# Optimization experiments

Measured on AMD Instinct MI355X. Metric: run time of the kernel, lower is better.

Reference implementation:

```python
import jax, jax.numpy as jnp
import numpy as np

W_CHAMFER = (1.0, 1.0, 1.0)
W_LAPLACE = 0.5
W_MOVE = 0.1
W_EDGE = 0.1
W_NORMAL = 1.6e-4
W_CONST = 1.0
LAP_CONST = (0.2, 1.0, 1.0)
EPS = 1e-12


def _normalize(x):
    # F.normalize(x, dim=-1): x / max(||x||, eps)
    n = jnp.sqrt(jnp.sum(x * x, axis=-1, keepdims=True))
    return x / jnp.maximum(n, EPS)


def _pairwise_sq(x, y):
    # x: (B,N,3), y: (B,M,3) -> (B,N,M) squared distances, GEMM form
    x2 = jnp.sum(x * x, -1)
    y2 = jnp.sum(y * y, -1)
    xy = jnp.einsum('bnd,bmd->bnm', x, y)
    return x2[:, :, None] + y2[:, None, :] - 2.0 * xy


def _laplace_coord(pts, lap_idx):
    # pts: (B,V,3); lap_idx: (V,10) = [8 neighbor idx (-1 invalid), self, count]
    idx = lap_idx[:, :8]
    mask = idx < 0
    safe = jnp.where(mask, 0, idx)
    nbrs = pts[:, safe]                                  # (B,V,8,3)
    nbrs = jnp.where(mask[None, :, :, None], 0.0, nbrs)
    count = lap_idx[:, -1].astype(pts.dtype)
    return pts - nbrs.sum(2) / count[None, :, None]


def setup_inputs():
    key = jax.random.key(0)
    B, M = 2, 8192
    Vs = (642, 2562, 10242)
    Es = (1920, 7680, 30720)
    ks = jax.random.split(key, 3 + 4 * 3)
    inp = {}
    inp['gt_coord'] = jax.random.normal(ks[0], (B, M, 3), jnp.float32)
    inp['gt_normal'] = _normalize(jax.random.normal(ks[1], (B, M, 3), jnp.float32))
    for i, (V, E) in enumerate(zip(Vs, Es)):
        k0, k1, k2, k3 = ks[3 + 4 * i], ks[4 + 4 * i], ks[5 + 4 * i], ks[6 + 4 * i]
        inp[f'pred_coord_{i}'] = jax.random.normal(k0, (B, V, 3), jnp.float32)
        inp[f'pred_before_{i}'] = inp[f'pred_coord_{i}'] + 0.05 * jax.random.normal(k1, (B, V, 3), jnp.float32)
        inp[f'edges_{i}'] = jax.random.randint(k2, (E, 2), 0, V)
        nbr = jax.random.randint(k3, (V, 8), 0, V)
        nbr = nbr.at[:, 6:].set(-1)                      # 6 valid neighbors, 2 invalid slots
        self_idx = jnp.arange(V)[:, None]
        count = jnp.full((V, 1), 6)
        inp[f'laplace_idx_{i}'] = jnp.concatenate([nbr, self_idx, count], axis=1)
    return inp


def reference(pred_coord_0, pred_coord_1, pred_coord_2, pred_before_0, pred_before_1, pred_before_2, gt_coord, gt_normal, laplace_idx_0, laplace_idx_1, laplace_idx_2, edges_0, edges_1, edges_2):
    preds = (pred_coord_0, pred_coord_1, pred_coord_2)
    befores = (pred_before_0, pred_before_1, pred_before_2)
    laps = (laplace_idx_0, laplace_idx_1, laplace_idx_2)
    edges_all = (edges_0, edges_1, edges_2)
    chamfer_loss = 0.0
    edge_loss = 0.0
    normal_loss = 0.0
    lap_loss = 0.0
    move_loss = 0.0
    for i in range(3):
        pred, before, lap_idx, edges = preds[i], befores[i], laps[i], edges_all[i]
        # shared pairwise distance matrix for chamfer + knn (original recomputes)
        d = _pairwise_sq(pred, gt_coord)                 # (B,V,M)
        chamfer_loss = chamfer_loss + W_CHAMFER[i] * (jnp.mean(jnp.min(d, axis=1)) + jnp.mean(jnp.min(d, axis=2)))
        knn_idx = jnp.argmin(d, axis=2)                  # (B,V): nearest gt per pred pt
        e0, e1 = edges[:, 0], edges[:, 1]
        evec = _normalize(pred[:, e0] - pred[:, e1])     # (B,E,3)
        # faithful to torch: knn.idx.flatten() then index_select -> only batch-0
        # indices ever selected since edge ids < V
        sel = knn_idx.reshape(-1)[e0]
        nrm = _normalize(gt_normal[:, sel])              # (B,E,3)
        normal_loss = normal_loss + jnp.mean(jnp.abs(jnp.sum(evec * nrm, axis=2)))
        edge_loss = edge_loss + 3.0 * jnp.mean((pred[:, e0] - pred[:, e1]) ** 2)
        l1 = _laplace_coord(before, lap_idx)
        l2 = _laplace_coord(pred, lap_idx)
        lap_loss = lap_loss + LAP_CONST[i] * 3.0 * jnp.mean((l1 - l2) ** 2)
        if i > 0:
            move_loss = move_loss + LAP_CONST[i] * 3.0 * jnp.mean((before - pred) ** 2)
    loss = chamfer_loss + W_LAPLACE * lap_loss + W_MOVE * move_loss + W_EDGE * edge_loss + W_NORMAL * normal_loss
    return W_CONST * loss
```

## Files before the change

kernel.cpp:

```cpp
#include <hip/hip_runtime.h>


#define DEV __device__ __forceinline__

DEV unsigned int ford(float f) {
    unsigned int u = __float_as_uint(f);
    return (u & 0x80000000u) ? ~u : (u | 0x80000000u);
}
DEV float funord(unsigned int o) {
    unsigned int u = (o & 0x80000000u) ? (o ^ 0x80000000u) : ~o;
    return __uint_as_float(u);
}
DEV unsigned long long umin64(unsigned long long a, unsigned long long b) { return a < b ? a : b; }

DEV float blockReduceSum256(float v) {
    #pragma unroll
    for (int o = 32; o > 0; o >>= 1) v += __shfl_down(v, o, 64);
    __shared__ float red4[4];
    int wid = threadIdx.x >> 6;
    if ((threadIdx.x & 63) == 0) red4[wid] = v;
    __syncthreads();
    return (threadIdx.x == 0) ? (red4[0] + red4[1] + red4[2] + red4[3]) : 0.0f;
}

template<bool STORE, bool ARGMIN>
DEV void roleA(int a, const float* p0, const float* p1, const float* p2,
               const float* gt, char* ws, char* smem)
{
    const int b = ARGMIN ? 0 : 1;
    int vtG = a >> 5, mc = a & 31;
    int lvl, vtL, V; const float* predL;
    if (vtG == 0)      { lvl = 0; vtL = 0;       V = 642;   predL = p0; }
    else if (vtG < 4)  { lvl = 1; vtL = vtG - 1; V = 2562;  predL = p1; }
    else               { lvl = 2; vtL = vtG - 4; V = 10242; predL = p2; }
    int tid = threadIdx.x, lane = tid & 63, w = tid >> 6;
    float4* SG = (float4*)smem;
    int mbase = mc << 8;
    {
        int m = mbase + tid;
        const float* gp = gt + ((size_t)b * 8192 + m) * 3;
        float gx = gp[0], gy = gp[1], gz = gp[2];
        SG[tid] = make_float4(-2.f * gx, -2.f * gy, -2.f * gz, fmaf(gx, gx, fmaf(gy, gy, gz * gz)));
    }
    float px[14], py[14], pz[14];
    #pragma unroll
    for (int r = 0; r < 14; r++) {
        int vr = vtL * 896 + r * 64 + lane;
        int v = vr - (vr >= V ? V : 0);
        const float* pp = predL + ((size_t)b * V + v) * 3;
        px[r] = pp[0]; py[r] = pp[1]; pz[r] = pp[2];
    }
    __syncthreads();
    if (ARGMIN) {
        float best[14]; int bi[14];
        #pragma unroll
        for (int r = 0; r < 14; r++) { best[r] = 3.0e38f; bi[r] = 0; }
        #pragma unroll 4
        for (int i = 0; i < 64; i++) {
            int j = (w << 6) + i;
            float4 q = SG[j];
            int cand = mbase + j;
            #pragma unroll
            for (int r = 0; r < 14; r++) {
                float d = fmaf(q.x, px[r], fmaf(q.y, py[r], fmaf(q.z, pz[r], q.w)));
                if (d < best[r]) { best[r] = d; bi[r] = cand; }
            }
        }
        unsigned long long* RED = (unsigned long long*)(smem + 4096);
        #pragma unroll
        for (int r = 0; r < 14; r++)
            RED[w * 896 + r * 64 + lane] = ((unsigned long long)ford(best[r]) << 32) | (unsigned)bi[r];
        __syncthreads();
        for (int s = tid; s < 896; s += 256) {
            unsigned long long mm = umin64(umin64(RED[s], RED[s + 896]),
                                           umin64(RED[s + 1792], RED[s + 2688]));
            if (STORE) {
                ((unsigned long long*)(ws + 54808))[((size_t)(vtG * 896 + s)) * 32 + mc] = mm;
            } else {
                int vr = vtL * 896 + s; int v = vr - (vr >= V ? V : 0);
                int lvlOff = (lvl == 0) ? 0 : (lvl == 1 ? 642 : 3204);
                atomicMin((unsigned long long*)(ws + 54808) + (lvlOff + v), mm);
            }
        }
    } else {
        float best[14];
        #pragma unroll
        for (int r = 0; r < 14; r++) best[r] = 3.0e38f;
        #pragma unroll 2
        for (int i = 0; i < 64; i += 2) {
            int j = (w << 6) + i;
            float4 q0 = SG[j], q1 = SG[j + 1];
            #pragma unroll
            for (int r = 0; r < 14; r++) {
                float d0 = fmaf(q0.x, px[r], fmaf(q0.y, py[r], fmaf(q0.z, pz[r], q0.w)));
                float d1 = fmaf(q1.x, px[r], fmaf(q1.y, py[r], fmaf(q1.z, pz[r], q1.w)));
                best[r] = fminf(fminf(best[r], d0), d1);
            }
        }
        unsigned* RED = (unsigned*)(smem + 4096);
        #pragma unroll
        for (int r = 0; r < 14; r++)
            RED[w * 896 + r * 64 + lane] = ford(best[r]);
        __syncthreads();
        for (int s = tid; s < 896; s += 256) {
            unsigned mm = min(min(RED[s], RED[s + 896]), min(RED[s + 1792], RED[s + 2688]));
            if (STORE) {
                ((unsigned*)(ws + 3724824))[((size_t)(vtG * 896 + s)) * 32 + mc] = mm;
            } else {
                int vr = vtL * 896 + s; int v = vr - (vr >= V ? V : 0);
                int lvlOff = (lvl == 0) ? 0 : (lvl == 1 ? 642 : 3204);
                atomicMin((unsigned*)(ws + 162376) + (lvlOff + v), mm);
            }
        }
    }
}

template<bool STORE>
DEV void roleB(int i, const float* p0, const float* p1, const float* p2,
               const float* gt, char* ws, char* smem)
{
    int lvl, V, cc, t, lvlB, baseB;
    if (i < 32)       { lvl = 0; V = 642;   cc = 2;  t = i;       lvlB = 0;     baseB = 0; }
    else if (i < 128) { lvl = 1; V = 2562;  cc = 6;  t = i - 32;  lvlB = 16384; baseB = 32768; }
    else              { lvl = 2; V = 10242; cc = 21; t = i - 128; lvlB = 32768; baseB = 131072; }
    const float* predL = lvl == 0 ? p0 : (lvl == 1 ? p1 : p2);
    int c = t % cc; int rest = t / cc; int mt = rest & 7; int b = rest >> 3;
    int tid = threadIdx.x, lane = tid & 63, w = tid >> 6;
    float4* SP = (float4*)smem;
    int vbase = c * 512;
    #pragma unroll
    for (int k = 0; k < 2; k++) {
        int j = tid + k * 256, v = vbase + j;
        if (v < V) {
            const float* pp = predL + ((size_t)b * V + v) * 3;
            float x = pp[0], y = pp[1], z = pp[2];
            SP[j] = make_float4(-2.f * x, -2.f * y, -2.f * z, fmaf(x, x, fmaf(y, y, z * z)));
        } else SP[j] = make_float4(0.f, 0.f, 0.f, 3.0e38f);
    }
    float gx[16], gy[16], gz[16];
    #pragma unroll
    for (int r = 0; r < 16; r++) {
        int m = mt * 1024 + r * 64 + lane;
        const float* gp = gt + ((size_t)b * 8192 + m) * 3;
        gx[r] = gp[0]; gy[r] = gp[1]; gz[r] = gp[2];
    }
    __syncthreads();
    float best[16];
    #pragma unroll
    for (int r = 0; r < 16; r++) best[r] = 3.0e38f;
    #pragma unroll 2
    for (int i2 = 0; i2 < 128; i2 += 2) {
        int j = (w << 7) + i2;
        float4 q0 = SP[j], q1 = SP[j + 1];
        #pragma unroll
        for (int r = 0; r < 16; r++) {
            float d0 = fmaf(q0.x, gx[r], fmaf(q0.y, gy[r], fmaf(q0.z, gz[r], q0.w)));
            float d1 = fmaf(q1.x, gx[r], fmaf(q1.y, gy[r], fmaf(q1.z, gz[r], q1.w)));
            best[r] = fminf(fminf(best[r], d0), d1);
        }
    }
    unsigned* RED = (unsigned*)(smem + 8192);
    #pragma unroll
    for (int r = 0; r < 16; r++)
        RED[w * 1024 + r * 64 + lane] = ford(best[r]);
    __syncthreads();
    for (int s = tid; s < 1024; s += 256) {
        unsigned mm = min(min(RED[s], RED[s + 1024]), min(RED[s + 2048], RED[s + 3072]));
        int m = mt * 1024 + s;
        if (STORE) ((unsigned*)(ws + 5559832))[baseB + (size_t)((b << 13) + m) * cc + c] = mm;
        else       atomicMin((unsigned*)(ws + 216160) + (lvlB + (b << 13) + m), mm);
    }
}

template<bool STORE>
__global__ __launch_bounds__(256, 3) void kMega(
    const float* __restrict__ p0, const float* __restrict__ p1, const float* __restrict__ p2,
    const float* __restrict__ b0p, const float* __restrict__ b1p, const float* __restrict__ b2p,
    const int* __restrict__ l0, const int* __restrict__ l1, const int* __restrict__ l2,
    const float* __restrict__ gt, char* ws)
{
    extern __shared__ char smem[];
    int bid = blockIdx.x;
    if (bid == 0 && threadIdx.x == 0) { *(float*)ws = 0.f; *(unsigned*)(ws + 4) = 0u; }
    if (bid < 128) {
        float c = 0.0f;
        int idx = bid * 256 + threadIdx.x;
        if (idx < 26892) {
            int level, V, t;
            const float *pred, *bef; const int* lap;
            if (idx < 1284)      { level = 0; V = 642;   pred = p0; bef = b0p; lap = l0; t = idx; }
            else if (idx < 6408) { level = 1; V = 2562;  pred = p1; bef = b1p; lap = l1; t = idx - 1284; }
            else                 { level = 2; V = 10242; pred = p2; bef = b2p; lap = l2; t = idx - 6408; }
            int b = t / V;
            int v = t - b * V;
            const float* P  = pred + ((size_t)b * V + v) * 3;
            const float* Bf = bef  + ((size_t)b * V + v) * 3;
            float dx = Bf[0] - P[0], dy = Bf[1] - P[1], dz = Bf[2] - P[2];
            float sx = 0.f, sy = 0.f, sz = 0.f;
            const int* L = lap + v * 10;
            #pragma unroll
            for (int j = 0; j < 8; j++) {
                int n = L[j];
                if (n >= 0) {
                    const float* Pn = pred + ((size_t)b * V + n) * 3;
                    const float* Bn = bef  + ((size_t)b * V + n) * 3;
                    sx += Bn[0] - Pn[0]; sy += Bn[1] - Pn[1]; sz += Bn[2] - Pn[2];
                }
            }
            float invc = 1.0f / (float)L[9];
            float lx = dx - sx * invc, ly = dy - sy * invc, lz = dz - sz * invc;
            float sl = fmaf(lx, lx, fmaf(ly, ly, lz * lz));
            float sm = fmaf(dx, dx, fmaf(dy, dy, dz * dz));
            float lapc = (level == 0) ? 0.2f : 1.0f;
            float iBV = 1.0f / (2.0f * (float)V);
            c = sl * (0.5f * lapc * iBV) + ((level > 0) ? sm * (0.1f * lapc * iBV) : 0.0f);
        }
        c = blockReduceSum256(c);
        if (threadIdx.x == 0) ((float*)(ws + 8))[bid] = c;
    }
    else if (bid < 592)  roleB<STORE>(bid - 128, p0, p1, p2, gt, ws, smem);
    else if (bid < 1104) roleA<STORE, true >(bid - 592,  p0, p1, p2, gt, ws, smem);
    else                 roleA<STORE, false>(bid - 1104, p0, p1, p2, gt, ws, smem);
}

template<bool STORE>
__global__ __launch_bounds__(256) void kCombine(
    const float* __restrict__ p0, const float* __restrict__ p1, const float* __restrict__ p2,
    const float* __restrict__ gt, char* ws)
{
    int bid = blockIdx.x, tid = threadIdx.x;
    float c = 0.0f;
    if (bid == 304) {
        if (tid < 128) c = ((float*)(ws + 8))[tid];
    } else {
        int idx = bid * 256 + tid;
        if (idx < 28672) {
            int b = idx / 14336;
            int q = idx % 14336;
            int vtG = q / 896, s = q % 896;
            int lvl, vtL, V; const float* predL; int lvlOff; float inv;
            if (vtG == 0)     { lvl = 0; vtL = 0;       V = 642;   predL = p0; lvlOff = 0;    inv = 1.f / 1284.f; }
            else if (vtG < 4) { lvl = 1; vtL = vtG - 1; V = 2562;  predL = p1; lvlOff = 642;  inv = 1.f / 5124.f; }
            else              { lvl = 2; vtL = vtG - 4; V = 10242; predL = p2; lvlOff = 3204; inv = 1.f / 20484.f; }
            int vr = vtL * 896 + s;
            if (vr < V) {
                float d; unsigned idxm = 0;
                if (STORE) {
                    if (b == 0) {
                        const unsigned long long* P = (const unsigned long long*)(ws + 54808)
                                                      + ((size_t)(vtG * 896 + s)) * 32;
                        unsigned long long mm = ~0ull;
                        #pragma unroll 8
                        for (int k = 0; k < 32; k++) mm = umin64(mm, P[k]);
                        d = funord((unsigned)(mm >> 32)); idxm = (unsigned)mm;
                    } else {
                        const unsigned* P = (const unsigned*)(ws + 3724824)
                                            + ((size_t)(vtG * 896 + s)) * 32;
                        unsigned mm = 0xFFFFFFFFu;
                        #pragma unroll 8
                        for (int k = 0; k < 32; k++) mm = min(mm, P[k]);
                        d = funord(mm);
                    }
                } else {
                    if (b == 0) {
                        unsigned long long mm = ((unsigned long long*)(ws + 54808))[lvlOff + vr];
                        d = funord((unsigned)(mm >> 32)); idxm = (unsigned)mm;
                    } else {
                        d = funord(((unsigned*)(ws + 162376))[lvlOff + vr]);
                    }
                }
                const float* pp = predL + ((size_t)b * V + vr) * 3;
                c = (d + fmaf(pp[0], pp[0], fmaf(pp[1], pp[1], pp[2] * pp[2]))) * inv;
                if (b == 0) ((int*)(ws + 1024))[lvlOff + vr] = (int)idxm;
            }
        } else if (idx < 77824) {
            int jj = idx - 28672;
            int lvl = jj >> 14, r = jj & 16383;
            int cc = lvl == 0 ? 2 : (lvl == 1 ? 6 : 21);
            int baseB = lvl == 0 ? 0 : (lvl == 1 ? 32768 : 131072);
            float d;
            if (STORE) {
                const unsigned* P = (const unsigned*)(ws + 5559832) + baseB + (size_t)r * cc;
                unsigned mm = 0xFFFFFFFFu;
                for (int k = 0; k < cc; k++) mm = min(mm, P[k]);
                d = funord(mm);
            } else {
                d = funord(((const unsigned*)(ws + 216160))[(lvl << 14) + r]);
            }
            const float* gp = gt + (size_t)r * 3;
            c = (d + fmaf(gp[0], gp[0], fmaf(gp[1], gp[1], gp[2] * gp[2]))) * (1.f / 16384.f);
        }
    }
    c = blockReduceSum256(c);
    if (tid == 0) atomicAdd((float*)ws, c);
}

__global__ __launch_bounds__(256) void kEdgeOut(
    const float* __restrict__ p0, const float* __restrict__ p1, const float* __restrict__ p2,
    const int* __restrict__ e0p, const int* __restrict__ e1p, const int* __restrict__ e2p,
    const float* __restrict__ gtn, char* ws, float* __restrict__ out)
{
    const int* knn = (const int*)(ws + 1024);
    int idx = blockIdx.x * 256 + threadIdx.x;
    float c = 0.0f;
    {
        int E, V, lvlOff, t;
        const float* pred; const int* edges;
        if (idx < 3840)       { E = 1920;  V = 642;   lvlOff = 0;    pred = p0; edges = e0p; t = idx; }
        else if (idx < 19200) { E = 7680;  V = 2562;  lvlOff = 642;  pred = p1; edges = e1p; t = idx - 3840; }
        else                  { E = 30720; V = 10242; lvlOff = 3204; pred = p2; edges = e2p; t = idx - 19200; }
        int b = t / E;
        int e = t % E;
        int a0 = edges[e * 2 + 0];
        int a1 = edges[e * 2 + 1];
        const float* P = pred + (size_t)b * V * 3;
        float dx = P[a0 * 3 + 0] - P[a1 * 3 + 0];
        float dy = P[a0 * 3 + 1] - P[a1 * 3 + 1];
        float dz = P[a0 * 3 + 2] - P[a1 * 3 + 2];
        float sq = fmaf(dx, dx, fmaf(dy, dy, dz * dz));
        float inv = 1.0f / fmaxf(sqrtf(sq), 1e-12f);
        int sel = knn[lvlOff + a0];
        const float* nr = gtn + ((size_t)b * 8192 + sel) * 3;
        float nx = nr[0], ny = nr[1], nz = nr[2];
        float invn = 1.0f / fmaxf(sqrtf(fmaf(nx, nx, fmaf(ny, ny, nz * nz))), 1e-12f);
        float dotv = fmaf(dx, nx, fmaf(dy, ny, dz * nz)) * inv * invn;
        float iBE = 1.0f / (2.0f * (float)E);
        c = sq * (0.1f * iBE) + fabsf(dotv) * (0.00016f * iBE);
    }
    c = blockReduceSum256(c);
    if (threadIdx.x == 0) {
        atomicAdd((float*)ws, c);
        __threadfence();
        unsigned t = atomicAdd((unsigned*)(ws + 4), 1u);
        if (t == 314u) out[0] = atomicAdd((float*)ws, 0.0f);
    }
}

extern "C" void kernel_launch(void* const* d_in, const int* in_sizes, int n_in,
                              void* d_out, int out_size, void* d_ws, size_t ws_size,
                              hipStream_t stream) {
    const float *gt, *gtn, *pred[3], *bef[3];
    const int *edg[3], *lapx[3];
    if (in_sizes[0] == 49152) {
        gt  = (const float*)d_in[0];
        gtn = (const float*)d_in[1];
        for (int i = 0; i < 3; i++) {
            pred[i] = (const float*)d_in[2 + 4 * i];
            bef[i]  = (const float*)d_in[3 + 4 * i];
            edg[i]  = (const int*)  d_in[4 + 4 * i];
            lapx[i] = (const int*)  d_in[5 + 4 * i];
        }
    } else {
        for (int i = 0; i < 3; i++) pred[i] = (const float*)d_in[i];
        for (int i = 0; i < 3; i++) bef[i]  = (const float*)d_in[3 + i];
        gt  = (const float*)d_in[6];
        gtn = (const float*)d_in[7];
        for (int i = 0; i < 3; i++) lapx[i] = (const int*)d_in[8 + i];
        for (int i = 0; i < 3; i++) edg[i]  = (const int*)d_in[11 + i];
    }

    char* ws = (char*)d_ws;
    bool store = ws_size >= (size_t)7460376;

    if (store) {
        kMega<true><<<1616, 256, 32768, stream>>>(pred[0], pred[1], pred[2],
                                                  bef[0], bef[1], bef[2],
                                                  lapx[0], lapx[1], lapx[2], gt, ws);
        kCombine<true><<<305, 256, 0, stream>>>(pred[0], pred[1], pred[2], gt, ws);
    } else {
        hipMemsetAsync(ws + 54808, 0xFF, 412768 - 54808, stream);
        kMega<false><<<1616, 256, 32768, stream>>>(pred[0], pred[1], pred[2],
                                                   bef[0], bef[1], bef[2],
                                                   lapx[0], lapx[1], lapx[2], gt, ws);
        kCombine<false><<<305, 256, 0, stream>>>(pred[0], pred[1], pred[2], gt, ws);
    }
    kEdgeOut<<<315, 256, 0, stream>>>(pred[0], pred[1], pred[2],
                                      edg[0], edg[1], edg[2], gtn, ws, (float*)d_out);
}
```

Before: 140.0 us.

## Use atomicMin reductions, merge combine and edge kernels, shrink roleB tiles

Drops the per-chunk partial-min store path and always reduces nearest distances with global atomicMin into a compact buffer. Folds the chamfer combine and edge/normal loss into one final kernel that reads the argmin index straight from the packed 64-bit min. roleB tiles get smaller (256 pred points), which yields more blocks, and the reduction scratch reuses the shared tile, lowering LDS so four blocks fit per CU. The cost is more atomic traffic and two memsets, in exchange for one fewer launch and less workspace traffic.

```diff
diff --git a/kernel.cpp b/kernel.cpp
--- a/kernel.cpp
+++ b/kernel.cpp
@@ -3,12 +3,18 @@
 
 #define DEV __device__ __forceinline__
 
-DEV unsigned int ford(float f) {
-    unsigned int u = __float_as_uint(f);
+#define OFF_LAP  8
+#define OFF_MA0  1024
+#define OFF_MA1  108592
+#define OFF_MB   162376
+#define MINS_END 358984
+
+DEV unsigned ford(float f) {
+    unsigned u = __float_as_uint(f);
     return (u & 0x80000000u) ? ~u : (u | 0x80000000u);
 }
-DEV float funord(unsigned int o) {
-    unsigned int u = (o & 0x80000000u) ? (o ^ 0x80000000u) : ~o;
+DEV float funord(unsigned o) {
+    unsigned u = (o & 0x80000000u) ? (o ^ 0x80000000u) : ~o;
     return __uint_as_float(u);
 }
 DEV unsigned long long umin64(unsigned long long a, unsigned long long b) { return a < b ? a : b; }
@@ -23,31 +29,31 @@
     return (threadIdx.x == 0) ? (red4[0] + red4[1] + red4[2] + red4[3]) : 0.0f;
 }
 
-template<bool STORE, bool ARGMIN>
+template<bool ARGMIN>
 DEV void roleA(int a, const float* p0, const float* p1, const float* p2,
                const float* gt, char* ws, char* smem)
 {
     const int b = ARGMIN ? 0 : 1;
     int vtG = a >> 5, mc = a & 31;
-    int lvl, vtL, V; const float* predL;
-    if (vtG == 0)      { lvl = 0; vtL = 0;       V = 642;   predL = p0; }
-    else if (vtG < 4)  { lvl = 1; vtL = vtG - 1; V = 2562;  predL = p1; }
-    else               { lvl = 2; vtL = vtG - 4; V = 10242; predL = p2; }
+    int vtL, V, lvlOff; const float* predL;
+    if (vtG == 0)     { vtL = 0;       V = 642;   predL = p0; lvlOff = 0; }
+    else if (vtG < 4) { vtL = vtG - 1; V = 2562;  predL = p1; lvlOff = 642; }
+    else              { vtL = vtG - 4; V = 10242; predL = p2; lvlOff = 3204; }
     int tid = threadIdx.x, lane = tid & 63, w = tid >> 6;
     float4* SG = (float4*)smem;
     int mbase = mc << 8;
     {
-        int m = mbase + tid;
-        const float* gp = gt + ((size_t)b * 8192 + m) * 3;
+        const float* gp = gt + ((size_t)(b * 8192 + mbase + tid)) * 3;
         float gx = gp[0], gy = gp[1], gz = gp[2];
-        SG[tid] = make_float4(-2.f * gx, -2.f * gy, -2.f * gz, fmaf(gx, gx, fmaf(gy, gy, gz * gz)));
+        SG[tid] = make_float4(-2.f * gx, -2.f * gy, -2.f * gz,
+                              fmaf(gx, gx, fmaf(gy, gy, gz * gz)));
     }
     float px[14], py[14], pz[14];
     #pragma unroll
     for (int r = 0; r < 14; r++) {
         int vr = vtL * 896 + r * 64 + lane;
         int v = vr - (vr >= V ? V : 0);
-        const float* pp = predL + ((size_t)b * V + v) * 3;
+        const float* pp = predL + ((size_t)(b * V + v)) * 3;
         px[r] = pp[0]; py[r] = pp[1]; pz[r] = pp[2];
     }
     __syncthreads();
@@ -66,21 +72,18 @@
                 if (d < best[r]) { best[r] = d; bi[r] = cand; }
             }
         }
-        unsigned long long* RED = (unsigned long long*)(smem + 4096);
+        __syncthreads();
+        unsigned long long* RED = (unsigned long long*)smem;
         #pragma unroll
         for (int r = 0; r < 14; r++)
             RED[w * 896 + r * 64 + lane] = ((unsigned long long)ford(best[r]) << 32) | (unsigned)bi[r];
         __syncthreads();
+        unsigned long long* MA0 = (unsigned long long*)(ws + OFF_MA0);
         for (int s = tid; s < 896; s += 256) {
             unsigned long long mm = umin64(umin64(RED[s], RED[s + 896]),
                                            umin64(RED[s + 1792], RED[s + 2688]));
-            if (STORE) {
-                ((unsigned long long*)(ws + 54808))[((size_t)(vtG * 896 + s)) * 32 + mc] = mm;
-            } else {
-                int vr = vtL * 896 + s; int v = vr - (vr >= V ? V : 0);
-                int lvlOff = (lvl == 0) ? 0 : (lvl == 1 ? 642 : 3204);
-                atomicMin((unsigned long long*)(ws + 54808) + (lvlOff + v), mm);
-            }
+            int vr = vtL * 896 + s; int v = vr - (vr >= V ? V : 0);
+            atomicMin(&MA0[lvlOff + v], mm);
         }
     } else {
         float best[14];
@@ -94,54 +97,49 @@
             for (int r = 0; r < 14; r++) {
                 float d0 = fmaf(q0.x, px[r], fmaf(q0.y, py[r], fmaf(q0.z, pz[r], q0.w)));
                 float d1 = fmaf(q1.x, px[r], fmaf(q1.y, py[r], fmaf(q1.z, pz[r], q1.w)));
-                best[r] = fminf(fminf(best[r], d0), d1);
+                best[r] = fminf(best[r], fminf(d0, d1));
             }
         }
-        unsigned* RED = (unsigned*)(smem + 4096);
+        __syncthreads();
+        unsigned* RED = (unsigned*)smem;
         #pragma unroll
         for (int r = 0; r < 14; r++)
             RED[w * 896 + r * 64 + lane] = ford(best[r]);
         __syncthreads();
+        unsigned* MA1 = (unsigned*)(ws + OFF_MA1);
         for (int s = tid; s < 896; s += 256) {
             unsigned mm = min(min(RED[s], RED[s + 896]), min(RED[s + 1792], RED[s + 2688]));
-            if (STORE) {
-                ((unsigned*)(ws + 3724824))[((size_t)(vtG * 896 + s)) * 32 + mc] = mm;
-            } else {
-                int vr = vtL * 896 + s; int v = vr - (vr >= V ? V : 0);
-                int lvlOff = (lvl == 0) ? 0 : (lvl == 1 ? 642 : 3204);
-                atomicMin((unsigned*)(ws + 162376) + (lvlOff + v), mm);
-            }
-        }
-    }
-}
-
-template<bool STORE>
+            int vr = vtL * 896 + s; int v = vr - (vr >= V ? V : 0);
+            atomicMin(&MA1[lvlOff + v], mm);
+        }
+    }
+}
+
 DEV void roleB(int i, const float* p0, const float* p1, const float* p2,
                const float* gt, char* ws, char* smem)
 {
-    int lvl, V, cc, t, lvlB, baseB;
-    if (i < 32)       { lvl = 0; V = 642;   cc = 2;  t = i;       lvlB = 0;     baseB = 0; }
-    else if (i < 128) { lvl = 1; V = 2562;  cc = 6;  t = i - 32;  lvlB = 16384; baseB = 32768; }
-    else              { lvl = 2; V = 10242; cc = 21; t = i - 128; lvlB = 32768; baseB = 131072; }
-    const float* predL = lvl == 0 ? p0 : (lvl == 1 ? p1 : p2);
-    int c = t % cc; int rest = t / cc; int mt = rest & 7; int b = rest >> 3;
+    int c55 = i % 55; int rest = i / 55; int mt = rest & 7; int b = rest >> 3;
+    int lvl, c, V; const float* predL;
+    if (c55 < 3)       { lvl = 0; c = c55;      V = 642;   predL = p0; }
+    else if (c55 < 14) { lvl = 1; c = c55 - 3;  V = 2562;  predL = p1; }
+    else               { lvl = 2; c = c55 - 14; V = 10242; predL = p2; }
     int tid = threadIdx.x, lane = tid & 63, w = tid >> 6;
     float4* SP = (float4*)smem;
-    int vbase = c * 512;
-    #pragma unroll
-    for (int k = 0; k < 2; k++) {
-        int j = tid + k * 256, v = vbase + j;
+    int vbase = c << 8;
+    {
+        int v = vbase + tid;
         if (v < V) {
-            const float* pp = predL + ((size_t)b * V + v) * 3;
+            const float* pp = predL + ((size_t)(b * V + v)) * 3;
             float x = pp[0], y = pp[1], z = pp[2];
-            SP[j] = make_float4(-2.f * x, -2.f * y, -2.f * z, fmaf(x, x, fmaf(y, y, z * z)));
-        } else SP[j] = make_float4(0.f, 0.f, 0.f, 3.0e38f);
+            SP[tid] = make_float4(-2.f * x, -2.f * y, -2.f * z,
+                                  fmaf(x, x, fmaf(y, y, z * z)));
+        } else SP[tid] = make_float4(0.f, 0.f, 0.f, 3.0e38f);
     }
     float gx[16], gy[16], gz[16];
     #pragma unroll
     for (int r = 0; r < 16; r++) {
-        int m = mt * 1024 + r * 64 + lane;
-        const float* gp = gt + ((size_t)b * 8192 + m) * 3;
+        int m = (mt << 10) + r * 64 + lane;
+        const float* gp = gt + ((size_t)(b * 8192 + m)) * 3;
         gx[r] = gp[0]; gy[r] = gp[1]; gz[r] = gp[2];
     }
     __syncthreads();
@@ -149,31 +147,30 @@
     #pragma unroll
     for (int r = 0; r < 16; r++) best[r] = 3.0e38f;
     #pragma unroll 2
-    for (int i2 = 0; i2 < 128; i2 += 2) {
-        int j = (w << 7) + i2;
+    for (int i2 = 0; i2 < 64; i2 += 2) {
+        int j = (w << 6) + i2;
         float4 q0 = SP[j], q1 = SP[j + 1];
         #pragma unroll
         for (int r = 0; r < 16; r++) {
             float d0 = fmaf(q0.x, gx[r], fmaf(q0.y, gy[r], fmaf(q0.z, gz[r], q0.w)));
             float d1 = fmaf(q1.x, gx[r], fmaf(q1.y, gy[r], fmaf(q1.z, gz[r], q1.w)));
-            best[r] = fminf(fminf(best[r], d0), d1);
-        }
-    }
-    unsigned* RED = (unsigned*)(smem + 8192);
+            best[r] = fminf(best[r], fminf(d0, d1));
+        }
+    }
+    __syncthreads();
+    unsigned* RED = (unsigned*)smem;
     #pragma unroll
     for (int r = 0; r < 16; r++)
-        RED[w * 1024 + r * 64 + lane] = ford(best[r]);
-    __syncthreads();
+        RED[(w << 10) + r * 64 + lane] = ford(best[r]);
+    __syncthreads();
+    unsigned* MB = (unsigned*)(ws + OFF_MB);
     for (int s = tid; s < 1024; s += 256) {
         unsigned mm = min(min(RED[s], RED[s + 1024]), min(RED[s + 2048], RED[s + 3072]));
-        int m = mt * 1024 + s;
-        if (STORE) ((unsigned*)(ws + 5559832))[baseB + (size_t)((b << 13) + m) * cc + c] = mm;
-        else       atomicMin((unsigned*)(ws + 216160) + (lvlB + (b << 13) + m), mm);
-    }
-}
-
-template<bool STORE>
-__global__ __launch_bounds__(256, 3) void kMega(
+        atomicMin(&MB[(lvl << 14) + (b << 13) + (mt << 10) + s], mm);
+    }
+}
+
+__global__ __launch_bounds__(256, 4) void kMega(
     const float* __restrict__ p0, const float* __restrict__ p1, const float* __restrict__ p2,
     const float* __restrict__ b0p, const float* __restrict__ b1p, const float* __restrict__ b2p,
     const int* __restrict__ l0, const int* __restrict__ l1, const int* __restrict__ l2,
@@ -181,7 +178,6 @@
 {
     extern __shared__ char smem[];
     int bid = blockIdx.x;
-    if (bid == 0 && threadIdx.x == 0) { *(float*)ws = 0.f; *(unsigned*)(ws + 4) = 0u; }
     if (bid < 128) {
         float c = 0.0f;
         int idx = bid * 256 + threadIdx.x;
@@ -216,94 +212,47 @@
             c = sl * (0.5f * lapc * iBV) + ((level > 0) ? sm * (0.1f * lapc * iBV) : 0.0f);
         }
         c = blockReduceSum256(c);
-        if (threadIdx.x == 0) ((float*)(ws + 8))[bid] = c;
-    }
-    else if (bid < 592)  roleB<STORE>(bid - 128, p0, p1, p2, gt, ws, smem);
-    else if (bid < 1104) roleA<STORE, true >(bid - 592,  p0, p1, p2, gt, ws, smem);
-    else                 roleA<STORE, false>(bid - 1104, p0, p1, p2, gt, ws, smem);
-}
-
-template<bool STORE>
-__global__ __launch_bounds__(256) void kCombine(
+        if (threadIdx.x == 0) ((float*)(ws + OFF_LAP))[bid] = c;
+    }
+    else if (bid < 1008) roleB(bid - 128, p0, p1, p2, gt, ws, smem);
+    else if (bid < 1520) roleA<true >(bid - 1008, p0, p1, p2, gt, ws, smem);
+    else                 roleA<false>(bid - 1520, p0, p1, p2, gt, ws, smem);
+}
+
+__global__ __launch_bounds__(256) void kFinal(
     const float* __restrict__ p0, const float* __restrict__ p1, const float* __restrict__ p2,
-    const float* __restrict__ gt, char* ws)
+    const int* __restrict__ e0p, const int* __restrict__ e1p, const int* __restrict__ e2p,
+    const float* __restrict__ gt, const float* __restrict__ gtn,
+    char* ws, float* __restrict__ out)
 {
     int bid = blockIdx.x, tid = threadIdx.x;
+    const unsigned long long* MA0 = (const unsigned long long*)(ws + OFF_MA0);
+    const unsigned* MA1 = (const unsigned*)(ws + OFF_MA1);
+    const unsigned* MB  = (const unsigned*)(ws + OFF_MB);
     float c = 0.0f;
-    if (bid == 304) {
-        if (tid < 128) c = ((float*)(ws + 8))[tid];
+    if (bid < 106) {
+        int idx = bid * 256 + tid;
+        if (idx < 26892) {
+            int b = idx >= 13446 ? 1 : 0;
+            int s = idx - (b ? 13446 : 0);
+            int v, V; const float* predL; float inv;
+            if (s < 642)       { v = s;        V = 642;   predL = p0; inv = 1.f / 1284.f; }
+            else if (s < 3204) { v = s - 642;  V = 2562;  predL = p1; inv = 1.f / 5124.f; }
+            else               { v = s - 3204; V = 10242; predL = p2; inv = 1.f / 20484.f; }
+            float d = b ? funord(MA1[s]) : funord((unsigned)(MA0[s] >> 32));
+            const float* pp = predL + ((size_t)(b * V + v)) * 3;
+            c = (d + fmaf(pp[0], pp[0], fmaf(pp[1], pp[1], pp[2] * pp[2]))) * inv;
+        }
+    } else if (bid < 298) {
+        int idx = (bid - 106) * 256 + tid;
+        int r = idx & 16383;
+        float d = funord(MB[idx]);
+        const float* gp = gt + (size_t)r * 3;
+        c = (d + fmaf(gp[0], gp[0], fmaf(gp[1], gp[1], gp[2] * gp[2]))) * (1.f / 16384.f);
+    } else if (bid == 298) {
+        if (tid < 128) c = ((const float*)(ws + OFF_LAP))[tid];
     } else {
-        int idx = bid * 256 + tid;
-        if (idx < 28672) {
-            int b = idx / 14336;
-            int q = idx % 14336;
-            int vtG = q / 896, s = q % 896;
-            int lvl, vtL, V; const float* predL; int lvlOff; float inv;
-            if (vtG == 0)     { lvl = 0; vtL = 0;       V = 642;   predL = p0; lvlOff = 0;    inv = 1.f / 1284.f; }
-            else if (vtG < 4) { lvl = 1; vtL = vtG - 1; V = 2562;  predL = p1; lvlOff = 642;  inv = 1.f / 5124.f; }
-            else              { lvl = 2; vtL = vtG - 4; V = 10242; predL = p2; lvlOff = 3204; inv = 1.f / 20484.f; }
-            int vr = vtL * 896 + s;
-            if (vr < V) {
-                float d; unsigned idxm = 0;
-                if (STORE) {
-                    if (b == 0) {
-                        const unsigned long long* P = (const unsigned long long*)(ws + 54808)
-                                                      + ((size_t)(vtG * 896 + s)) * 32;
-                        unsigned long long mm = ~0ull;
-                        #pragma unroll 8
-                        for (int k = 0; k < 32; k++) mm = umin64(mm, P[k]);
-                        d = funord((unsigned)(mm >> 32)); idxm = (unsigned)mm;
-                    } else {
-                        const unsigned* P = (const unsigned*)(ws + 3724824)
-                                            + ((size_t)(vtG * 896 + s)) * 32;
-                        unsigned mm = 0xFFFFFFFFu;
-                        #pragma unroll 8
-                        for (int k = 0; k < 32; k++) mm = min(mm, P[k]);
-                        d = funord(mm);
-                    }
-                } else {
-                    if (b == 0) {
-                        unsigned long long mm = ((unsigned long long*)(ws + 54808))[lvlOff + vr];
-                        d = funord((unsigned)(mm >> 32)); idxm = (unsigned)mm;
-                    } else {
-                        d = funord(((unsigned*)(ws + 162376))[lvlOff + vr]);
-                    }
-                }
-                const float* pp = predL + ((size_t)b * V + vr) * 3;
-                c = (d + fmaf(pp[0], pp[0], fmaf(pp[1], pp[1], pp[2] * pp[2]))) * inv;
-                if (b == 0) ((int*)(ws + 1024))[lvlOff + vr] = (int)idxm;
-            }
-        } else if (idx < 77824) {
-            int jj = idx - 28672;
-            int lvl = jj >> 14, r = jj & 16383;
-            int cc = lvl == 0 ? 2 : (lvl == 1 ? 6 : 21);
-            int baseB = lvl == 0 ? 0 : (lvl == 1 ? 32768 : 131072);
-            float d;
-            if (STORE) {
-                const unsigned* P = (const unsigned*)(ws + 5559832) + baseB + (size_t)r * cc;
-                unsigned mm = 0xFFFFFFFFu;
-                for (int k = 0; k < cc; k++) mm = min(mm, P[k]);
-                d = funord(mm);
-            } else {
-                d = funord(((const unsigned*)(ws + 216160))[(lvl << 14) + r]);
-            }
-            const float* gp = gt + (size_t)r * 3;
-            c = (d + fmaf(gp[0], gp[0], fmaf(gp[1], gp[1], gp[2] * gp[2]))) * (1.f / 16384.f);
-        }
-    }
-    c = blockReduceSum256(c);
-    if (tid == 0) atomicAdd((float*)ws, c);
-}
-
-__global__ __launch_bounds__(256) void kEdgeOut(
-    const float* __restrict__ p0, const float* __restrict__ p1, const float* __restrict__ p2,
-    const int* __restrict__ e0p, const int* __restrict__ e1p, const int* __restrict__ e2p,
-    const float* __restrict__ gtn, char* ws, float* __restrict__ out)
-{
-    const int* knn = (const int*)(ws + 1024);
-    int idx = blockIdx.x * 256 + threadIdx.x;
-    float c = 0.0f;
-    {
+        int idx = (bid - 299) * 256 + tid;
         int E, V, lvlOff, t;
         const float* pred; const int* edges;
         if (idx < 3840)       { E = 1920;  V = 642;   lvlOff = 0;    pred = p0; edges = e0p; t = idx; }
@@ -319,7 +268,7 @@
         float dz = P[a0 * 3 + 2] - P[a1 * 3 + 2];
         float sq = fmaf(dx, dx, fmaf(dy, dy, dz * dz));
         float inv = 1.0f / fmaxf(sqrtf(sq), 1e-12f);
-        int sel = knn[lvlOff + a0];
+        int sel = (int)(unsigned)MA0[lvlOff + a0];
         const float* nr = gtn + ((size_t)b * 8192 + sel) * 3;
         float nx = nr[0], ny = nr[1], nz = nr[2];
         float invn = 1.0f / fmaxf(sqrtf(fmaf(nx, nx, fmaf(ny, ny, nz * nz))), 1e-12f);
@@ -328,11 +277,11 @@
         c = sq * (0.1f * iBE) + fabsf(dotv) * (0.00016f * iBE);
     }
     c = blockReduceSum256(c);
-    if (threadIdx.x == 0) {
+    if (tid == 0) {
         atomicAdd((float*)ws, c);
         __threadfence();
         unsigned t = atomicAdd((unsigned*)(ws + 4), 1u);
-        if (t == 314u) out[0] = atomicAdd((float*)ws, 0.0f);
+        if (t == gridDim.x - 1) out[0] = atomicAdd((float*)ws, 0.0f);
     }
 }
 
@@ -360,20 +309,13 @@
     }
 
     char* ws = (char*)d_ws;
-    bool store = ws_size >= (size_t)7460376;
-
-    if (store) {
-        kMega<true><<<1616, 256, 32768, stream>>>(pred[0], pred[1], pred[2],
-                                                  bef[0], bef[1], bef[2],
-                                                  lapx[0], lapx[1], lapx[2], gt, ws);
-        kCombine<true><<<305, 256, 0, stream>>>(pred[0], pred[1], pred[2], gt, ws);
-    } else {
-        hipMemsetAsync(ws + 54808, 0xFF, 412768 - 54808, stream);
-        kMega<false><<<1616, 256, 32768, stream>>>(pred[0], pred[1], pred[2],
-                                                   bef[0], bef[1], bef[2],
-                                                   lapx[0], lapx[1], lapx[2], gt, ws);
-        kCombine<false><<<305, 256, 0, stream>>>(pred[0], pred[1], pred[2], gt, ws);
-    }
-    kEdgeOut<<<315, 256, 0, stream>>>(pred[0], pred[1], pred[2],
-                                      edg[0], edg[1], edg[2], gtn, ws, (float*)d_out);
-}
+    hipMemsetAsync(ws, 0, 8, stream);
+    hipMemsetAsync(ws + OFF_MA0, 0xFF, MINS_END - OFF_MA0, stream);
+
+    kMega<<<2032, 256, 28672, stream>>>(pred[0], pred[1], pred[2],
+                                        bef[0], bef[1], bef[2],
+                                        lapx[0], lapx[1], lapx[2], gt, ws);
+    kFinal<<<614, 256, 0, stream>>>(pred[0], pred[1], pred[2],
+                                    edg[0], edg[1], edg[2], gt, gtn,
+                                    ws, (float*)d_out);
+}
```

Measured after the change: 145.5 us. 1.04x slower.
